# Kernel tuning notes

Measured on AMD Instinct MI355X. Metric: run time of the kernel, lower is better.

Reference implementation:

```python
import jax, jax.numpy as jnp
import numpy as np

# Hardcoded competition weights from the original module (8 targets: 7 vertebrae + overall)
W_NEG = jnp.array([1, 1, 1, 1, 1, 1, 1, 7], dtype=jnp.float32)
W_POS = jnp.array([2, 2, 2, 2, 2, 2, 2, 14], dtype=jnp.float32)
EPS = 1e-8


def setup_inputs() -> dict:
    key = jax.random.key(0)
    k1, k2 = jax.random.split(key)
    N, C = 2_000_000, 8
    # logits are probabilities in (0,1): log(p) and log(1-p) are both taken
    logits = jax.random.uniform(k1, (N, C), dtype=jnp.float32, minval=1e-3, maxval=1.0 - 1e-3)
    # binary 0/1 labels as float
    targets = (jax.random.uniform(k2, (N, C), dtype=jnp.float32) < 0.5).astype(jnp.float32)
    return {"logits": logits, "targets": targets}


def reference(logits, targets):
    # per-element weight: y*w_pos + (1-y)*w_neg  (broadcast over rows)
    w = targets * W_POS + (1.0 - targets) * W_NEG
    # weighted BCE per element (vectorized form of the original double loop)
    L = -w * (targets * jnp.log(logits + EPS) + (1.0 - targets) * jnp.log(1.0 - logits + EPS))
    # per-exam loss: weighted mean over the 8 targets
    return jnp.sum(L, axis=1) / jnp.sum(w, axis=1)
```

## Files before the change

### kernel.cpp

```cpp
#include <hip/hip_runtime.h>
#include <hip/hip_bf16.h>


#define EPS 1e-8f

__global__ __launch_bounds__(256) void densenet_loss_kernel(
        const float4* __restrict__ logits,
        const float4* __restrict__ targets,
        float* __restrict__ out,
        int n) {
    int row = blockIdx.x * blockDim.x + threadIdx.x;
    if (row >= n) return;

    float4 l0 = logits[2 * row + 0];
    float4 l1 = logits[2 * row + 1];
    float4 t0 = targets[2 * row + 0];
    float4 t1 = targets[2 * row + 1];

    const float l[8] = {l0.x, l0.y, l0.z, l0.w, l1.x, l1.y, l1.z, l1.w};
    const float t[8] = {t0.x, t0.y, t0.z, t0.w, t1.x, t1.y, t1.z, t1.w};
    const float wneg[8] = {1.f, 1.f, 1.f, 1.f, 1.f, 1.f, 1.f, 7.f};
    const float wpos[8] = {2.f, 2.f, 2.f, 2.f, 2.f, 2.f, 2.f, 14.f};

    float num = 0.f;
    float den = 0.f;
#pragma unroll
    for (int c = 0; c < 8; ++c) {
        float ti = t[c];
        float w  = ti * wpos[c] + (1.f - ti) * wneg[c];
        float lp = __logf(l[c] + EPS);
        float lq = __logf(1.f - l[c] + EPS);
        num += w * (ti * lp + (1.f - ti) * lq);
        den += w;
    }
    out[row] = -num / den;
}

extern "C" void kernel_launch(void* const* d_in, const int* in_sizes, int n_in,
                              void* d_out, int out_size, void* d_ws, size_t ws_size,
                              hipStream_t stream) {
    const float4* logits  = (const float4*)d_in[0];
    const float4* targets = (const float4*)d_in[1];
    float* out = (float*)d_out;

    int n = in_sizes[0] / 8;
    int block = 256;
    int grid = (n + block - 1) / block;
    densenet_loss_kernel<<<grid, block, 0, stream>>>(logits, targets, out, n);
}
```

Measured before the change: 25.55 us.

## Split each row across two threads with float4 loads and shuffle-reduce

Each thread now handles half a row (one float4 of logits and targets), so adjacent lanes read contiguous float4s and global loads are fully coalesced instead of strided by 32 bytes. The two half-row partial sums are combined with a lane shuffle, and the even lane writes the result. The loss math is also simplified to one log per element, choosing log(p) or log(1-p) by the label, which assumes labels are exactly 0 or 1. This doubles the thread count and adds a shuffle, and only even lanes issue the output store.

```diff
diff --git a/kernel.cpp b/kernel.cpp
--- a/kernel.cpp
+++ b/kernel.cpp
@@ -8,32 +8,34 @@
         const float4* __restrict__ logits,
         const float4* __restrict__ targets,
         float* __restrict__ out,
-        int n) {
-    int row = blockIdx.x * blockDim.x + threadIdx.x;
-    if (row >= n) return;
+        int n4) {
+    int j = blockIdx.x * blockDim.x + threadIdx.x;
+    if (j >= n4) return;
 
-    float4 l0 = logits[2 * row + 0];
-    float4 l1 = logits[2 * row + 1];
-    float4 t0 = targets[2 * row + 0];
-    float4 t1 = targets[2 * row + 1];
+    float4 l4 = logits[j];
+    float4 t4 = targets[j];
 
-    const float l[8] = {l0.x, l0.y, l0.z, l0.w, l1.x, l1.y, l1.z, l1.w};
-    const float t[8] = {t0.x, t0.y, t0.z, t0.w, t1.x, t1.y, t1.z, t1.w};
-    const float wneg[8] = {1.f, 1.f, 1.f, 1.f, 1.f, 1.f, 1.f, 7.f};
-    const float wpos[8] = {2.f, 2.f, 2.f, 2.f, 2.f, 2.f, 2.f, 14.f};
+    const float lv[4] = {l4.x, l4.y, l4.z, l4.w};
+    const float tv[4] = {t4.x, t4.y, t4.z, t4.w};
+
+    const bool hi = (j & 1);
 
     float num = 0.f;
     float den = 0.f;
 #pragma unroll
-    for (int c = 0; c < 8; ++c) {
-        float ti = t[c];
-        float w  = ti * wpos[c] + (1.f - ti) * wneg[c];
-        float lp = __logf(l[c] + EPS);
-        float lq = __logf(1.f - l[c] + EPS);
-        num += w * (ti * lp + (1.f - ti) * lq);
+    for (int k = 0; k < 4; ++k) {
+        float base = (hi && k == 3) ? 7.f : 1.f;
+        float ti   = tv[k];
+        float w    = base * (1.f + ti);
+        float arg  = (ti > 0.5f) ? (lv[k] + EPS) : (1.f - lv[k] + EPS);
+        num += w * __logf(arg);
         den += w;
     }
-    out[row] = -num / den;
+
+    num += __shfl_xor(num, 1);
+    den += __shfl_xor(den, 1);
+
+    if (!hi) out[j >> 1] = -num / den;
 }
 
 extern "C" void kernel_launch(void* const* d_in, const int* in_sizes, int n_in,
@@ -43,8 +45,8 @@
     const float4* targets = (const float4*)d_in[1];
     float* out = (float*)d_out;
 
-    int n = in_sizes[0] / 8;
+    int n4 = in_sizes[0] / 4;
     int block = 256;
-    int grid = (n + block - 1) / block;
-    densenet_loss_kernel<<<grid, block, 0, stream>>>(logits, targets, out, n);
+    int grid = (n4 + block - 1) / block;
+    densenet_loss_kernel<<<grid, block, 0, stream>>>(logits, targets, out, n4);
 }
```

New measurement: 25.41 us. No clear change (-0.5%).
